# Optimization experiments

Hardware: AMD Instinct MI355X
Metric: run time of the kernel (lower is better)

The kernel has to match this reference:

```python
import jax, jax.numpy as jnp
import numpy as np

N = 100000
E = 3200000
IN_CH = 128


def gcn_conv(x, src, dst, W, b, n):
    # x' = D^{-1/2} (A + I) D^{-1/2} x W + b  (PyG GCNConv defaults)
    h = x @ W  # [N, out]
    ones = jnp.ones(src.shape[0], dtype=h.dtype)
    deg = jax.ops.segment_sum(ones, dst, num_segments=n)  # in-degree incl. self-loops
    dinv = jnp.where(deg > 0, jax.lax.rsqrt(deg), 0.0)
    norm = dinv[src] * dinv[dst]  # [E+N]
    msg = h[src] * norm[:, None]  # gather + scale
    out = jax.ops.segment_sum(msg, dst, num_segments=n)  # scatter-add
    return out + b


def setup_inputs() -> dict:
    key = jax.random.key(0)
    ks = jax.random.split(key, 16)
    x = jax.random.normal(ks[0], (N, IN_CH), dtype=jnp.float32)
    edge_index = jax.random.randint(ks[1], (2, E), 0, N, dtype=jnp.int64)

    def lin(kw, kb, fan_in, fan_out):
        bound = 1.0 / np.sqrt(fan_in)
        W = jax.random.uniform(kw, (fan_in, fan_out), jnp.float32, -bound, bound)
        b = jax.random.uniform(kb, (fan_out,), jnp.float32, -bound, bound)
        return W, b

    W1, b1 = lin(ks[2], ks[3], IN_CH, 64)
    W2, b2 = lin(ks[4], ks[5], 64, 64)
    lw1, lb1 = lin(ks[6], ks[7], 64, 64)
    lw2, lb2 = lin(ks[8], ks[9], 64, 32)
    lw3, lb3 = lin(ks[10], ks[11], 32, 1)
    return {"x": x, "edge_index": edge_index, "W1": W1, "b1": b1,
            "W2": W2, "b2": b2, "lw1": lw1, "lb1": lb1,
            "lw2": lw2, "lb2": lb2, "lw3": lw3, "lb3": lb3}


def reference(x, edge_index, W1, b1, W2, b2, lw1, lb1, lw2, lb2, lw3, lb3):
    n = x.shape[0]
    loop = jnp.arange(n, dtype=edge_index.dtype)
    src = jnp.concatenate([edge_index[0], loop])  # add self-loops
    dst = jnp.concatenate([edge_index[1], loop])
    h = gcn_conv(x, src, dst, W1, b1, n)
    h = gcn_conv(h, src, dst, W2, b2, n)
    h = jax.nn.relu(h @ lw1 + lb1)
    h = jax.nn.relu(h @ lw2 + lb2)
    return h @ lw3 + lb3
```

## Files before the change

kernel.cpp:

```cpp
#include <hip/hip_runtime.h>

#define IN_CH 128
#define HID 64
#define TILE 8192
#define B2SHIFT 10
#define B2NODES 1024

__global__ __launch_bounds__(256) void k_hist1(const int* __restrict__ dst,
                                               int* __restrict__ H, int E, int P) {
  __shared__ int cnt[1024];
  const int tid = threadIdx.x;
  for (int i = tid; i < P; i += 256) cnt[i] = 0;
  __syncthreads();
  const int base = blockIdx.x * TILE;
  const int end = min(base + TILE, E);
  for (int i = base + tid; i < end; i += 256)
    atomicAdd(&cnt[dst[i] >> B2SHIFT], 1);
  __syncthreads();
  for (int i = tid; i < P; i += 256) H[blockIdx.x * P + i] = cnt[i];
}

__global__ __launch_bounds__(256) void k_colscan(const int* __restrict__ H,
    int* __restrict__ Orel, int* __restrict__ colTot, int P, int NBLK) {
  __shared__ int s[512];
  const int b = blockIdx.x, tid = threadIdx.x;
  const int iA = tid, iB = tid + 256;
  int origA = (iA < NBLK) ? H[iA * P + b] : 0;
  int origB = (iB < NBLK) ? H[iB * P + b] : 0;
  s[iA] = origA; s[iB] = origB;
  __syncthreads();
  for (int off = 1; off < 512; off <<= 1) {
    int tA = (iA >= off) ? s[iA - off] : 0;
    int tB = (iB >= off) ? s[iB - off] : 0;
    __syncthreads();
    s[iA] += tA; s[iB] += tB;
    __syncthreads();
  }
  if (iA < NBLK) Orel[iA * P + b] = s[iA] - origA;
  if (iB < NBLK) Orel[iB * P + b] = s[iB] - origB;
  if (tid == 255) colTot[b] = s[511];
}

__global__ __launch_bounds__(128) void k_bbase(const int* __restrict__ colTot,
                                               int* __restrict__ bBase, int P) {
  __shared__ int s[128];
  const int tid = threadIdx.x;
  int v = (tid < P) ? colTot[tid] : 0;
  s[tid] = v;
  __syncthreads();
  for (int off = 1; off < 128; off <<= 1) {
    int t = (tid >= off) ? s[tid - off] : 0;
    __syncthreads();
    s[tid] += t;
    __syncthreads();
  }
  if (tid < P) bBase[tid] = s[tid] - v;
  if (tid == P - 1) bBase[P] = s[tid];
}

__global__ __launch_bounds__(256) void k_pass1b(const int* __restrict__ src,
    const int* __restrict__ dst, const int* __restrict__ Orel,
    const int* __restrict__ bBase, unsigned* __restrict__ pairBuf, int E, int P) {
  __shared__ int off[1024], cur[1024];
  const int tid = threadIdx.x;
  for (int i = tid; i < P; i += 256) {
    off[i] = bBase[i] + Orel[blockIdx.x * P + i];
    cur[i] = 0;
  }
  __syncthreads();
  const int base = blockIdx.x * TILE;
  const int end = min(base + TILE, E);
  for (int i = base + tid; i < end; i += 256) {
    int d = dst[i];
    int b = d >> B2SHIFT;
    int r = atomicAdd(&cur[b], 1);
    pairBuf[off[b] + r] = ((unsigned)(d & (B2NODES - 1)) << 17) | (unsigned)src[i];
  }
}

__global__ __launch_bounds__(256) void k_pass2(const unsigned* __restrict__ pairBuf,
    const int* __restrict__ bBase, int* __restrict__ csr, int* __restrict__ rowptr,
    int* __restrict__ degInt, float* __restrict__ dinv, int N) {
  __shared__ int cnt[B2NODES], pfx[B2NODES], cur[B2NODES];
  __shared__ int lsum[256];
  const int b = blockIdx.x, tid = threadIdx.x;
  const int e0 = bBase[b], e1 = bBase[b + 1];
  for (int i = tid; i < B2NODES; i += 256) { cnt[i] = 0; cur[i] = 0; }
  __syncthreads();
  for (int i = e0 + tid; i < e1; i += 256)
    atomicAdd(&cnt[pairBuf[i] >> 17], 1);
  __syncthreads();
  int v[4], tsum = 0;
  #pragma unroll
  for (int k = 0; k < 4; ++k) { v[k] = cnt[tid * 4 + k]; tsum += v[k]; }
  lsum[tid] = tsum;
  __syncthreads();
  for (int off = 1; off < 256; off <<= 1) {
    int t = (tid >= off) ? lsum[tid - off] : 0;
    __syncthreads();
    lsum[tid] += t;
    __syncthreads();
  }
  int run = lsum[tid] - tsum;
  #pragma unroll
  for (int k = 0; k < 4; ++k) { pfx[tid * 4 + k] = run; run += v[k]; }
  __syncthreads();
  #pragma unroll
  for (int k = 0; k < 4; ++k) {
    int l = tid * 4 + k;
    int node = (b << B2SHIFT) + l;
    if (node < N) {
      rowptr[node] = e0 + pfx[l];
      degInt[node] = cnt[l];
      dinv[node]   = 1.0f / sqrtf((float)cnt[l] + 1.0f);
    }
  }
  __syncthreads();
  for (int i = e0 + tid; i < e1; i += 256) {
    unsigned u = pairBuf[i];
    int dl = u >> 17;
    int r = atomicAdd(&cur[dl], 1);
    csr[e0 + pfx[dl] + r] = (int)(u & 0x1FFFFu);
  }
}

__global__ __launch_bounds__(256) void k_gemm1(const float* __restrict__ x,
    const float* __restrict__ W1, const float* __restrict__ dinv,
    float* __restrict__ g1, int N) {
  __shared__ __align__(16) float Ws[IN_CH * HID];
  __shared__ __align__(16) float xs[64 * IN_CH];
  const int tid = threadIdx.x;
  const int base = blockIdx.x * 64;
  for (int i = tid; i < IN_CH * HID; i += 256) Ws[i] = W1[i];
  for (int i = tid; i < 64 * IN_CH; i += 256) {
    int row = i >> 7, col = i & 127;
    int n = base + row; if (n > N - 1) n = N - 1;
    xs[(row << 7) + (col ^ (row & 3))] = x[(size_t)n * IN_CH + col];
  }
  __syncthreads();
  const int w = tid >> 6, lane = tid & 63;
  const int ng = lane >> 4, cg = lane & 15;
  float acc[4][4];
  #pragma unroll
  for (int j = 0; j < 4; ++j)
    #pragma unroll
    for (int c = 0; c < 4; ++c) acc[j][c] = 0.f;
  #pragma unroll 8
  for (int k = 0; k < IN_CH; ++k) {
    float4 wv = *(const float4*)&Ws[(k << 6) + (cg << 2)];
    #pragma unroll
    for (int j = 0; j < 4; ++j) {
      int row = w * 16 + j * 4 + ng;
      float xv = xs[(row << 7) + (k ^ ng)];
      acc[j][0] = fmaf(xv, wv.x, acc[j][0]);
      acc[j][1] = fmaf(xv, wv.y, acc[j][1]);
      acc[j][2] = fmaf(xv, wv.z, acc[j][2]);
      acc[j][3] = fmaf(xv, wv.w, acc[j][3]);
    }
  }
  #pragma unroll
  for (int j = 0; j < 4; ++j) {
    int node = base + w * 16 + j * 4 + ng;
    if (node < N) {
      float di = dinv[node];
      float4 gv;
      gv.x = acc[j][0] * di; gv.y = acc[j][1] * di;
      gv.z = acc[j][2] * di; gv.w = acc[j][3] * di;
      *(float4*)&g1[(size_t)node * HID + (cg << 2)] = gv;
    }
  }
}

__global__ __launch_bounds__(256) void k_gemm2(const float* __restrict__ accIn,
    const float* __restrict__ W2, const float* __restrict__ b1,
    const float* __restrict__ dinv,
    float* __restrict__ g2, int N) {
  __shared__ __align__(16) float Ws[HID * HID];
  __shared__ __align__(16) float vs[64 * HID];
  const int tid = threadIdx.x;
  const int base = blockIdx.x * 64;
  for (int i = tid; i < HID * HID; i += 256) Ws[i] = W2[i];
  for (int i = tid; i < 64 * HID; i += 256) {
    int row = i >> 6, col = i & 63;
    int n = base + row; if (n > N - 1) n = N - 1;
    float v = fmaf(accIn[(size_t)n * HID + col], dinv[n], b1[col]);
    vs[(row << 6) + (col ^ (row & 3))] = v;
  }
  __syncthreads();
  const int w = tid >> 6, lane = tid & 63;
  const int ng = lane >> 4, cg = lane & 15;
  float acc[4][4];
  #pragma unroll
  for (int j = 0; j < 4; ++j)
    #pragma unroll
    for (int c = 0; c < 4; ++c) acc[j][c] = 0.f;
  #pragma unroll 8
  for (int k = 0; k < HID; ++k) {
    float4 wv = *(const float4*)&Ws[(k << 6) + (cg << 2)];
    #pragma unroll
    for (int j = 0; j < 4; ++j) {
      int row = w * 16 + j * 4 + ng;
      float xv = vs[(row << 6) + (k ^ ng)];
      acc[j][0] = fmaf(xv, wv.x, acc[j][0]);
      acc[j][1] = fmaf(xv, wv.y, acc[j][1]);
      acc[j][2] = fmaf(xv, wv.z, acc[j][2]);
      acc[j][3] = fmaf(xv, wv.w, acc[j][3]);
    }
  }
  #pragma unroll
  for (int j = 0; j < 4; ++j) {
    int node = base + w * 16 + j * 4 + ng;
    if (node < N) {
      float di = dinv[node];
      float4 gv;
      gv.x = acc[j][0] * di; gv.y = acc[j][1] * di;
      gv.z = acc[j][2] * di; gv.w = acc[j][3] * di;
      *(float4*)&g2[(size_t)node * HID + (cg << 2)] = gv;
    }
  }
}

__global__ __launch_bounds__(256) void k_gather(const int* __restrict__ rowptr,
    const int* __restrict__ degInt, const int* __restrict__ csr,
    const float* __restrict__ g, float* __restrict__ out, int N) {
  const int lane = threadIdx.x & 63;
  const int wid = (blockIdx.x * 256 + threadIdx.x) >> 6;
  if (wid >= N) return;
  const int start = rowptr[wid];
  const int deg = degInt[wid];
  float sum = g[(size_t)wid * HID + lane];
  for (int c = 0; c < deg; c += 64) {
    int rem = deg - c;
    int cnt = rem < 64 ? rem : 64;
    int idx = 0;
    if (lane < cnt) idx = csr[start + c + lane];
    int j = 0;
    for (; j + 8 <= cnt; j += 8) {
      int s0 = __shfl(idx, j, 64);
      int s1 = __shfl(idx, j + 1, 64);
      int s2 = __shfl(idx, j + 2, 64);
      int s3 = __shfl(idx, j + 3, 64);
      int s4 = __shfl(idx, j + 4, 64);
      int s5 = __shfl(idx, j + 5, 64);
      int s6 = __shfl(idx, j + 6, 64);
      int s7 = __shfl(idx, j + 7, 64);
      float a0 = g[(size_t)s0 * HID + lane];
      float a1 = g[(size_t)s1 * HID + lane];
      float a2 = g[(size_t)s2 * HID + lane];
      float a3 = g[(size_t)s3 * HID + lane];
      float a4 = g[(size_t)s4 * HID + lane];
      float a5 = g[(size_t)s5 * HID + lane];
      float a6 = g[(size_t)s6 * HID + lane];
      float a7 = g[(size_t)s7 * HID + lane];
      sum += a0; sum += a1; sum += a2; sum += a3;
      sum += a4; sum += a5; sum += a6; sum += a7;
    }
    for (; j + 4 <= cnt; j += 4) {
      int s0 = __shfl(idx, j, 64);
      int s1 = __shfl(idx, j + 1, 64);
      int s2 = __shfl(idx, j + 2, 64);
      int s3 = __shfl(idx, j + 3, 64);
      float a0 = g[(size_t)s0 * HID + lane];
      float a1 = g[(size_t)s1 * HID + lane];
      float a2 = g[(size_t)s2 * HID + lane];
      float a3 = g[(size_t)s3 * HID + lane];
      sum += a0; sum += a1; sum += a2; sum += a3;
    }
    for (; j < cnt; ++j)
      sum += g[(size_t)__shfl(idx, j, 64) * HID + lane];
  }
  out[(size_t)wid * HID + lane] = sum;
}

__global__ __launch_bounds__(256) void k_mlp(const float* __restrict__ accIn,
    const float* __restrict__ dinv, const float* __restrict__ b2,
    const float* __restrict__ lw1, const float* __restrict__ lb1,
    const float* __restrict__ lw2, const float* __restrict__ lb2,
    const float* __restrict__ lw3, const float* __restrict__ lb3,
    float* __restrict__ out, int N) {
  __shared__ __align__(16) float w1s[64 * 64];
  __shared__ __align__(16) float w2s[64 * 32];
  __shared__ float w3s[32], b2s[64], lb1s[64], lb2s[32];
  __shared__ float vls[4][64], t1ls[4][64];
  const int tid = threadIdx.x;
  for (int i = tid; i < 4096; i += 256) w1s[i] = lw1[i];
  for (int i = tid; i < 2048; i += 256) w2s[i] = lw2[i];
  if (tid < 64) { b2s[tid] = b2[tid]; lb1s[tid] = lb1[tid]; }
  if (tid < 32) { w3s[tid] = lw3[tid]; lb2s[tid] = lb2[tid]; }
  const float lb3v = lb3[0];
  __syncthreads();
  const int w = tid >> 6, lane = tid & 63;
  const int base = blockIdx.x * 16;
  for (int rep = 0; rep < 4; ++rep) {
    int nd = base + w * 4 + rep;
    int node = nd < N ? nd : N - 1;
    float di = dinv[node];
    float v = fmaf(accIn[(size_t)node * HID + lane], di, b2s[lane]);
    vls[w][lane] = v;
    __syncthreads();
    float t1 = lb1s[lane];
    #pragma unroll
    for (int k = 0; k < 64; ++k) t1 = fmaf(vls[w][k], w1s[(k << 6) + lane], t1);
    t1 = fmaxf(t1, 0.f);
    t1ls[w][lane] = t1;
    __syncthreads();
    const int l2 = lane & 31;
    float t2 = lb2s[l2];
    #pragma unroll
    for (int k = 0; k < 64; ++k) t2 = fmaf(t1ls[w][k], w2s[(k << 5) + l2], t2);
    t2 = fmaxf(t2, 0.f);
    float p = (lane < 32) ? t2 * w3s[l2] : 0.f;
    #pragma unroll
    for (int m = 1; m < 64; m <<= 1) p += __shfl_xor(p, m, 64);
    if (lane == 0 && nd < N) out[nd] = p + lb3v;
    __syncthreads();
  }
}

extern "C" void kernel_launch(void* const* d_in, const int* in_sizes, int n_in,
                              void* d_out, int out_size, void* d_ws, size_t ws_size,
                              hipStream_t stream) {
  const float* x   = (const float*)d_in[0];
  const int*   ei  = (const int*)d_in[1];
  const float* W1  = (const float*)d_in[2];
  const float* b1  = (const float*)d_in[3];
  const float* W2  = (const float*)d_in[4];
  const float* b2  = (const float*)d_in[5];
  const float* lw1 = (const float*)d_in[6];
  const float* lb1 = (const float*)d_in[7];
  const float* lw2 = (const float*)d_in[8];
  const float* lb2 = (const float*)d_in[9];
  const float* lw3 = (const float*)d_in[10];
  const float* lb3 = (const float*)d_in[11];
  float* out = (float*)d_out;

  const int N = in_sizes[0] / IN_CH;
  const int E = in_sizes[1] / 2;
  const int* src = ei;
  const int* dst = ei + E;
  const int NBLK = (E + TILE - 1) / TILE;
  const int P = (N + B2NODES - 1) >> B2SHIFT;

  auto align256 = [](size_t v) { return (v + 255) & ~(size_t)255; };
  char* ws = (char*)d_ws;
  size_t nB = align256((size_t)N * 4);
  float* dinv   = (float*)ws;  ws += nB;
  int*   degInt = (int*)ws;    ws += nB;
  int*   rowptr = (int*)ws;    ws += nB;
  int*   H      = (int*)ws;    ws += align256((size_t)NBLK * P * 4);
  int*   Orel   = (int*)ws;    ws += align256((size_t)NBLK * P * 4);
  int*   colTot = (int*)ws;    ws += align256((size_t)P * 4);
  int*   bBase  = (int*)ws;    ws += align256((size_t)(P + 1) * 4);
  int*   csr    = (int*)ws;    ws += align256((size_t)E * 4);
  float* bufA   = (float*)ws;  ws += (size_t)N * HID * 4;
  float* bufB   = (float*)ws;
  unsigned* pairBuf = (unsigned*)bufB;

  const int gb  = (N + 63) / 64;
  const int gatherBlocks = (N * 64 + 255) / 256;

  hipLaunchKernelGGL(k_hist1,   dim3(NBLK), dim3(256), 0, stream, dst, H, E, P);
  hipLaunchKernelGGL(k_colscan, dim3(P), dim3(256), 0, stream, H, Orel, colTot, P, NBLK);
  hipLaunchKernelGGL(k_bbase,   dim3(1), dim3(128), 0, stream, colTot, bBase, P);
  hipLaunchKernelGGL(k_pass1b,  dim3(NBLK), dim3(256), 0, stream, src, dst, Orel, bBase, pairBuf, E, P);
  hipLaunchKernelGGL(k_pass2,   dim3(P), dim3(256), 0, stream, pairBuf, bBase,
                     csr, rowptr, degInt, dinv, N);

  hipLaunchKernelGGL(k_gemm1, dim3(gb), dim3(256), 0, stream, x, W1, dinv, bufA, N);
  hipLaunchKernelGGL(k_gather, dim3(gatherBlocks), dim3(256), 0, stream,
                     rowptr, degInt, csr, bufA, bufB, N);
  hipLaunchKernelGGL(k_gemm2, dim3(gb), dim3(256), 0, stream, bufB, W2, b1, dinv, bufA, N);
  hipLaunchKernelGGL(k_gather, dim3(gatherBlocks), dim3(256), 0, stream,
                     rowptr, degInt, csr, bufA, bufB, N);
  hipLaunchKernelGGL(k_mlp, dim3((N + 15) / 16), dim3(256), 0, stream,
                     bufB, dinv, b2, lw1, lb1, lw2, lb2, lw3, lb3, out, N);
}
```

Measured before the change: 598.1 us.

## Register-tile the final MLP kernel over 64 nodes per block

Rewrites the MLP head so each block stages 64 node rows into XOR-swizzled shared memory. Each thread then computes a 4x4 (and later 4x2) register tile using vectorized weight loads, instead of handling one node per wave with per-node barriers. This amortizes the shared-memory weight loads across more nodes and removes many __syncthreads, in exchange for more shared memory per block and higher register pressure. The launch grid changes to one block per 64 nodes.

New measurement: 538.4 us. -10.0%, faster.

```diff
diff --git a/kernel.cpp b/kernel.cpp
--- a/kernel.cpp
+++ b/kernel.cpp
@@ -280,40 +280,77 @@
     float* __restrict__ out, int N) {
   __shared__ __align__(16) float w1s[64 * 64];
   __shared__ __align__(16) float w2s[64 * 32];
-  __shared__ float w3s[32], b2s[64], lb1s[64], lb2s[32];
-  __shared__ float vls[4][64], t1ls[4][64];
-  const int tid = threadIdx.x;
+  __shared__ float w3s[32], lb1s[64], lb2s[32];
+  __shared__ __align__(16) float vs[64 * 64];
+  __shared__ __align__(16) float t1s[64 * 64];
+  const int tid = threadIdx.x;
+  const int base = blockIdx.x * 64;
   for (int i = tid; i < 4096; i += 256) w1s[i] = lw1[i];
   for (int i = tid; i < 2048; i += 256) w2s[i] = lw2[i];
-  if (tid < 64) { b2s[tid] = b2[tid]; lb1s[tid] = lb1[tid]; }
+  if (tid < 64) lb1s[tid] = lb1[tid];
   if (tid < 32) { w3s[tid] = lw3[tid]; lb2s[tid] = lb2[tid]; }
   const float lb3v = lb3[0];
+  for (int i = tid; i < 64 * 64; i += 256) {
+    int row = i >> 6, col = i & 63;
+    int n = base + row; if (n > N - 1) n = N - 1;
+    vs[(row << 6) + (col ^ (row & 3))] = fmaf(accIn[(size_t)n * HID + col], dinv[n], b2[col]);
+  }
   __syncthreads();
   const int w = tid >> 6, lane = tid & 63;
-  const int base = blockIdx.x * 16;
-  for (int rep = 0; rep < 4; ++rep) {
-    int nd = base + w * 4 + rep;
-    int node = nd < N ? nd : N - 1;
-    float di = dinv[node];
-    float v = fmaf(accIn[(size_t)node * HID + lane], di, b2s[lane]);
-    vls[w][lane] = v;
-    __syncthreads();
-    float t1 = lb1s[lane];
-    #pragma unroll
-    for (int k = 0; k < 64; ++k) t1 = fmaf(vls[w][k], w1s[(k << 6) + lane], t1);
-    t1 = fmaxf(t1, 0.f);
-    t1ls[w][lane] = t1;
-    __syncthreads();
-    const int l2 = lane & 31;
-    float t2 = lb2s[l2];
-    #pragma unroll
-    for (int k = 0; k < 64; ++k) t2 = fmaf(t1ls[w][k], w2s[(k << 5) + l2], t2);
-    t2 = fmaxf(t2, 0.f);
-    float p = (lane < 32) ? t2 * w3s[l2] : 0.f;
-    #pragma unroll
-    for (int m = 1; m < 64; m <<= 1) p += __shfl_xor(p, m, 64);
-    if (lane == 0 && nd < N) out[nd] = p + lb3v;
-    __syncthreads();
+  const int ng = lane >> 4, cg = lane & 15;
+  float acc[4][4];
+  #pragma unroll
+  for (int j = 0; j < 4; ++j)
+    #pragma unroll
+    for (int c = 0; c < 4; ++c) acc[j][c] = lb1s[(cg << 2) + c];
+  #pragma unroll 8
+  for (int k = 0; k < 64; ++k) {
+    float4 wv = *(const float4*)&w1s[(k << 6) + (cg << 2)];
+    #pragma unroll
+    for (int j = 0; j < 4; ++j) {
+      int row = w * 16 + j * 4 + ng;
+      float xv = vs[(row << 6) + (k ^ ng)];
+      acc[j][0] = fmaf(xv, wv.x, acc[j][0]);
+      acc[j][1] = fmaf(xv, wv.y, acc[j][1]);
+      acc[j][2] = fmaf(xv, wv.z, acc[j][2]);
+      acc[j][3] = fmaf(xv, wv.w, acc[j][3]);
+    }
+  }
+  #pragma unroll
+  for (int j = 0; j < 4; ++j) {
+    int row = w * 16 + j * 4 + ng;
+    #pragma unroll
+    for (int c = 0; c < 4; ++c)
+      t1s[(row << 6) + (((cg << 2) + c) ^ ng)] = fmaxf(acc[j][c], 0.f);
+  }
+  __syncthreads();
+  float a2[4][2];
+  #pragma unroll
+  for (int j = 0; j < 4; ++j) {
+    a2[j][0] = lb2s[(cg << 1)];
+    a2[j][1] = lb2s[(cg << 1) + 1];
+  }
+  #pragma unroll 8
+  for (int k = 0; k < 64; ++k) {
+    float2 wv = *(const float2*)&w2s[(k << 5) + (cg << 1)];
+    #pragma unroll
+    for (int j = 0; j < 4; ++j) {
+      int row = w * 16 + j * 4 + ng;
+      float xv = t1s[(row << 6) + (k ^ ng)];
+      a2[j][0] = fmaf(xv, wv.x, a2[j][0]);
+      a2[j][1] = fmaf(xv, wv.y, a2[j][1]);
+    }
+  }
+  const float w3a = w3s[(cg << 1)], w3b = w3s[(cg << 1) + 1];
+  #pragma unroll
+  for (int j = 0; j < 4; ++j) {
+    float p = fmaxf(a2[j][0], 0.f) * w3a + fmaxf(a2[j][1], 0.f) * w3b;
+    p += __shfl_xor(p, 1, 64);
+    p += __shfl_xor(p, 2, 64);
+    p += __shfl_xor(p, 4, 64);
+    p += __shfl_xor(p, 8, 64);
+    int node = base + w * 16 + j * 4 + ng;
+    if (cg == 0 && node < N) out[node] = p + lb3v;
   }
 }
 
@@ -372,6 +409,6 @@
   hipLaunchKernelGGL(k_gemm2, dim3(gb), dim3(256), 0, stream, bufB, W2, b1, dinv, bufA, N);
   hipLaunchKernelGGL(k_gather, dim3(gatherBlocks), dim3(256), 0, stream,
                      rowptr, degInt, csr, bufA, bufB, N);
-  hipLaunchKernelGGL(k_mlp, dim3((N + 15) / 16), dim3(256), 0, stream,
+  hipLaunchKernelGGL(k_mlp, dim3(gb), dim3(256), 0, stream,
                      bufB, dinv, b2, lw1, lb1, lw2, lb2, lw3, lb3, out, N);
 }
```
